# Performance work log

Measured on AMD Instinct MI355X. Metric: run time of the kernel, lower is better.

The kernel has to match this reference:

```python
import jax, jax.numpy as jnp
import numpy as np
from jax import lax

NC = 8  # num_classes
NUM_ITERS = 2


def _resize_bilinear_ac(x, out_h, out_w):
    """Bilinear resize with align_corners=True, x: (N, C, H, W)."""
    N, C, H, W = x.shape

    def coords(n_out, n_in):
        if n_out == 1:
            return jnp.zeros((1,), jnp.float32)
        return jnp.linspace(0.0, float(n_in - 1), n_out, dtype=jnp.float32)

    ys = coords(out_h, H)
    xs = coords(out_w, W)
    y0 = jnp.floor(ys).astype(jnp.int32)
    y1 = jnp.minimum(y0 + 1, H - 1)
    wy = (ys - y0.astype(jnp.float32)).astype(x.dtype)
    x0 = jnp.floor(xs).astype(jnp.int32)
    x1 = jnp.minimum(x0 + 1, W - 1)
    wx = (xs - x0.astype(jnp.float32)).astype(x.dtype)

    r0 = x[:, :, y0, :]
    r1 = x[:, :, y1, :]
    r = r0 * (1.0 - wy)[None, None, :, None] + r1 * wy[None, None, :, None]
    c0 = r[:, :, :, x0]
    c1 = r[:, :, :, x1]
    return c0 * (1.0 - wx)[None, None, None, :] + c1 * wx[None, None, None, :]


def _conv2d(x, w, groups=1):
    k = w.shape[-1]
    pad = k // 2
    return lax.conv_general_dilated(
        x, w, window_strides=(1, 1), padding=[(pad, pad), (pad, pad)],
        dimension_numbers=('NCHW', 'OIHW', 'NCHW'), feature_group_count=groups)


def _mean_field_update(unary, guidance, spatial_w, bilateral_w, compat_w):
    Q = jax.nn.softmax(unary, axis=1)
    cw = compat_w[:, :, 0, 0]  # (O, I)
    for _ in range(NUM_ITERS):
        spatial_msg = _conv2d(Q, spatial_w, groups=NC)          # depthwise 3x3
        bilateral_in = jnp.concatenate([Q, guidance], axis=1)   # (N, NC+6, H, W)
        bilateral_msg = _conv2d(bilateral_in, bilateral_w)      # 3x3 dense
        message = spatial_msg + bilateral_msg
        message = jnp.einsum('nchw,oc->nohw', message, cw)      # 1x1 compat conv
        Q = jax.nn.softmax(unary - message, axis=1)
    return Q


def setup_inputs() -> dict:
    key = jax.random.key(0)
    ks = jax.random.split(key, 16)
    inp = {
        'logits': jax.random.normal(ks[0], (8, NC, 512, 512), jnp.float32),
        'image': jax.random.uniform(ks[1], (8, 3, 512, 512), jnp.float32),
        'skip0': jax.random.normal(ks[2], (8, 64, 256, 256), jnp.float32),
        'skip1': jax.random.normal(ks[3], (8, 128, 128, 128), jnp.float32),
        'skip2': jax.random.normal(ks[4], (8, 256, 64, 64), jnp.float32),
        'skip3': jax.random.normal(ks[5], (8, 512, 32, 32), jnp.float32),
        'spatial_w': jax.random.normal(ks[6], (NC, 1, 3, 3), jnp.float32) * 0.1,
        'bilateral_w': jax.random.normal(ks[7], (NC, NC + 6, 3, 3), jnp.float32) * 0.1,
        # compat_conv is initialized to -I (zeros then -= eye) in the module
        'compat_w': (-jnp.eye(NC, dtype=jnp.float32)).reshape(NC, NC, 1, 1),
        'skip_w0': jax.random.normal(ks[8], (3, 64, 1, 1), jnp.float32) * 0.05,
        'skip_b0': jnp.zeros((3,), jnp.float32),
        'skip_w1': jax.random.normal(ks[9], (3, 128, 1, 1), jnp.float32) * 0.05,
        'skip_b1': jnp.zeros((3,), jnp.float32),
        'skip_w2': jax.random.normal(ks[10], (3, 256, 1, 1), jnp.float32) * 0.05,
        'skip_b2': jnp.zeros((3,), jnp.float32),
        'skip_w3': jax.random.normal(ks[11], (3, 512, 1, 1), jnp.float32) * 0.05,
        'skip_b3': jnp.zeros((3,), jnp.float32),
    }
    return inp


def reference(logits, image, skip0, skip1, skip2, skip3,
              spatial_w, bilateral_w, compat_w,
              skip_w0, skip_b0, skip_w1, skip_b1,
              skip_w2, skip_b2, skip_w3, skip_b3):
    H, W = logits.shape[2], logits.shape[3]

    # fuse_skip_features: 1x1 project each skip to 3ch, upsample, average
    skips = [skip0, skip1, skip2, skip3]
    ws = [skip_w0, skip_w1, skip_w2, skip_w3]
    bs = [skip_b0, skip_b1, skip_b2, skip_b3]
    fused = jnp.zeros((logits.shape[0], 3, H, W), logits.dtype)
    for feat, w, b in zip(skips, ws, bs):
        p = jnp.einsum('nchw,oc->nohw', feat, w[:, :, 0, 0]) + b[None, :, None, None]
        fused = fused + _resize_bilinear_ac(p, H, W)
    fused = fused / len(skips)

    guidance = jnp.concatenate([image, fused], axis=1)  # (N, 6, H, W)

    Q_full = _mean_field_update(logits, guidance, spatial_w, bilateral_w, compat_w)

    logits_down = _resize_bilinear_ac(logits, H // 2, W // 2)
    guidance_down = _resize_bilinear_ac(guidance, H // 2, W // 2)
    Q_down = _mean_field_update(logits_down, guidance_down, spatial_w, bilateral_w, compat_w)
    Q_down_up = _resize_bilinear_ac(Q_down, H, W)

    return (Q_full + Q_down_up) / 2.0
```

## Files before the change

kernel.cpp:

```cpp
#include <hip/hip_runtime.h>
#include <hip/hip_fp16.h>
#include <math.h>

#define NB 8
#define NCLS 8
#define NGU 6
#define NBI 14
#define HF 512
#define WF 512
#define HH 256
#define WH 256

#define TOX 32
#define TOY 16
#define SX 36
#define SY 20
#define SPX (SY * SX)
#define R1W 36
#define R1N (18 * 36)
#define R1T 41
#define R2T 32
#define PLANE (SPX * 8)
#define PSTR (PLANE + 32)
#define TILEH (16 + PSTR + PLANE + 16)

typedef _Float16 f16x8 __attribute__((ext_vector_type(8)));
typedef float f32x4 __attribute__((ext_vector_type(4)));

static __device__ __forceinline__ void ac_prep(int o, float scale, int insz,
                                               int& i0, int& i1, float& f) {
    float s = (float)o * scale;
    int ii = (int)floorf(s);
    if (ii > insz - 1) ii = insz - 1;
    if (ii < 0) ii = 0;
    i0 = ii;
    i1 = (ii + 1 < insz) ? (ii + 1) : (insz - 1);
    f = s - (float)ii;
}

static __device__ __forceinline__ void dma16(const _Float16* g, _Float16* l) {
    __builtin_amdgcn_global_load_lds(
        (const __attribute__((address_space(1))) void*)g,
        (__attribute__((address_space(3))) void*)l, 16, 0, 0);
}

__global__ __launch_bounds__(256) void k_init(
    float* __restrict__ p1, float* __restrict__ p2, float* __restrict__ p3,
    const float* __restrict__ b1, const float* __restrict__ b2, const float* __restrict__ b3,
    const float* __restrict__ wsp, const float* __restrict__ wbil,
    const float* __restrict__ cw, _Float16* __restrict__ wf) {
    int bid = blockIdx.x;
    int tid = threadIdx.x;
    if (bid < 2016) {
        int i = bid * 256 + tid;
        if (i < NB * 3 * 16384) { p1[i] = b1[(i / 16384) % 3]; return; }
        i -= NB * 3 * 16384;
        if (i < NB * 3 * 4096) { p2[i] = b2[(i / 4096) % 3]; return; }
        i -= NB * 3 * 4096;
        p3[i] = b3[(i / 1024) % 3];
        return;
    }
    __shared__ float sW2[NBI * 72];
    for (int i = tid; i < NBI * 72; i += 256) {
        int o = i & 7;
        int t = (i >> 3) % 9;
        int ci = i / 72;
        float s = 0.f;
        for (int c = 0; c < NCLS; ++c)
            s += cw[o * NCLS + c] * wbil[((size_t)c * NBI + ci) * 9 + t];
        if (ci < NCLS) s += cw[o * NCLS + ci] * wsp[ci * 9 + t];
        sW2[i] = s;
    }
    __syncthreads();
    for (int i = tid; i < 5 * 64; i += 256) {
        int l = i & 63;
        int col = l & 15, kg = l >> 4;
        #pragma unroll
        for (int e = 0; e < 8; ++e) {
            int k = (i >> 6) * 32 + kg * 8 + e;
            int tap = k >> 4, ci = k & 15;
            float v = (tap < 9 && ci < 14 && col < 8) ? sW2[ci * 72 + tap * 8 + col] : 0.f;
            wf[i * 8 + e] = (_Float16)v;
        }
    }
}

template <int VEC, int CH, bool DIRECT>
static __device__ __forceinline__ void skip_level(
    const float* __restrict__ feat, const float* __restrict__ sw,
    const float* __restrict__ bias, float* __restrict__ out,
    int C, int HW, int nch, int idx) {
    const int HWv = HW / VEC;
    int hv = idx % HWv;
    int t = idx / HWv;
    int ch = t % nch;
    int n = t / nch;
    int c0 = ch * CH;
    const float* fp = feat + ((size_t)n * C + c0) * HW + (size_t)hv * VEC;
    float a[3][VEC];
    #pragma unroll
    for (int o = 0; o < 3; ++o)
        #pragma unroll
        for (int k = 0; k < VEC; ++k) a[o][k] = 0.f;
    #pragma unroll 8
    for (int c = 0; c < CH; ++c) {
        float v[VEC];
        if constexpr (VEC == 2) {
            float2 t2 = *reinterpret_cast<const float2*>(fp + (size_t)c * HW);
            v[0] = t2.x; v[1] = t2.y;
        } else {
            v[0] = fp[(size_t)c * HW];
        }
        #pragma unroll
        for (int o = 0; o < 3; ++o) {
            const float wv = sw[o * C + c0 + c];
            #pragma unroll
            for (int k = 0; k < VEC; ++k) a[o][k] = fmaf(wv, v[k], a[o][k]);
        }
    }
    float* op = out + (size_t)n * 3 * HW + (size_t)hv * VEC;
    #pragma unroll
    for (int o = 0; o < 3; ++o) {
        #pragma unroll
        for (int k = 0; k < VEC; ++k) {
            if (DIRECT)
                op[(size_t)o * HW + k] = bias[o] + a[o][k];
            else
                atomicAdd(&op[(size_t)o * HW + k], a[o][k]);
        }
    }
}

__global__ __launch_bounds__(256) void k_skip_all(
    const float* __restrict__ s0, const float* __restrict__ s1,
    const float* __restrict__ s2, const float* __restrict__ s3,
    const float* __restrict__ w0, const float* __restrict__ w1,
    const float* __restrict__ w2, const float* __restrict__ w3,
    const float* __restrict__ b0,
    float* __restrict__ p0, float* __restrict__ p1,
    float* __restrict__ p2, float* __restrict__ p3) {
    __shared__ float sw[3 * 512];
    const int bid = blockIdx.x;
    const int lvl = bid >> 10;
    const int idx = (bid & 1023) * 256 + threadIdx.x;
    const float* w = (lvl == 0) ? w0 : (lvl == 1) ? w1 : (lvl == 2) ? w2 : w3;
    const int C = (lvl == 0) ? 64 : (lvl == 1) ? 128 : (lvl == 2) ? 256 : 512;
    for (int i = threadIdx.x; i < 3 * C; i += 256) sw[i] = w[i];
    __syncthreads();
    if (lvl == 0)      skip_level<2, 64, true >(s0, sw, b0, p0, 64, 65536, 1, idx);
    else if (lvl == 1) skip_level<2, 32, false>(s1, sw, nullptr, p1, 128, 16384, 4, idx);
    else if (lvl == 2) skip_level<1, 32, false>(s2, sw, nullptr, p2, 256, 4096, 8, idx);
    else               skip_level<1, 16, false>(s3, sw, nullptr, p3, 512, 1024, 32, idx);
}

__global__ void k_prep_full(const float* __restrict__ logits, const float* __restrict__ image,
                            const float* __restrict__ p0, const float* __restrict__ p1,
                            const float* __restrict__ p2, const float* __restrict__ p3,
                            _Float16* __restrict__ Gh, _Float16* __restrict__ Q0h) {
    const int HW = HF * WF;
    int t = blockIdx.x * blockDim.x + threadIdx.x;
    if (t >= NB * HW / 2) return;
    int idx = t * 2;
    int n = idx / HW, r = idx - n * HW;
    int y = r / WF, x = r - y * WF;

    const float* ps[4] = {p0, p1, p2, p3};
    const int ss[4] = {256, 128, 64, 32};
    float f[2][3] = {{0.f, 0.f, 0.f}, {0.f, 0.f, 0.f}};
    #pragma unroll
    for (int l = 0; l < 4; ++l) {
        int s = ss[l];
        float scale = (float)(s - 1) / 511.0f;
        int y0, y1;
        float fy;
        ac_prep(y, scale, s, y0, y1, fy);
        const float* pb = ps[l] + (size_t)n * 3 * s * s;
        #pragma unroll
        for (int k = 0; k < 2; ++k) {
            int x0, x1;
            float fx;
            ac_prep(x + k, scale, s, x0, x1, fx);
            #pragma unroll
            for (int o = 0; o < 3; ++o) {
                const float* pp = pb + (size_t)o * s * s;
                float v00 = pp[y0 * s + x0], v01 = pp[y0 * s + x1];
                float v10 = pp[y1 * s + x0], v11 = pp[y1 * s + x1];
                float r0 = v00 * (1.f - fy) + v10 * fy;
                float r1 = v01 * (1.f - fy) + v11 * fy;
                f[k][o] += r0 * (1.f - fx) + r1 * fx;
            }
        }
    }
    const float* ip = image + (size_t)n * 3 * HW + r;
    float2 img[3];
    #pragma unroll
    for (int o = 0; o < 3; ++o) img[o] = *reinterpret_cast<const float2*>(&ip[(size_t)o * HW]);
    const float* up = logits + (size_t)n * NCLS * HW + r;
    float2 u[8];
    #pragma unroll
    for (int o = 0; o < 8; ++o) u[o] = *reinterpret_cast<const float2*>(&up[(size_t)o * HW]);

    f16x8 gv[2], qv[2];
    #pragma unroll
    for (int k = 0; k < 2; ++k) {
        gv[k][0] = (_Float16)(k ? img[0].y : img[0].x);
        gv[k][1] = (_Float16)(k ? img[1].y : img[1].x);
        gv[k][2] = (_Float16)(k ? img[2].y : img[2].x);
        gv[k][3] = (_Float16)(f[k][0] * 0.25f);
        gv[k][4] = (_Float16)(f[k][1] * 0.25f);
        gv[k][5] = (_Float16)(f[k][2] * 0.25f);
        gv[k][6] = (_Float16)0.f;
        gv[k][7] = (_Float16)0.f;
        float e[8];
        float s = 0.f;
        #pragma unroll
        for (int o = 0; o < 8; ++o) { e[o] = __expf(k ? u[o].y : u[o].x); s += e[o]; }
        float inv = 1.f / s;
        #pragma unroll
        for (int o = 0; o < 8; ++o) qv[k][o] = (_Float16)(e[o] * inv);
    }
    *(f16x8*)(Gh + (size_t)idx * 8) = gv[0];
    *(f16x8*)(Gh + (size_t)idx * 8 + 8) = gv[1];
    *(f16x8*)(Q0h + (size_t)idx * 8) = qv[0];
    *(f16x8*)(Q0h + (size_t)idx * 8 + 8) = qv[1];
}

template <bool DOWN, bool UPFOLD>
__global__ __launch_bounds__(256, 4) void k_mf_mfma(
    const float* __restrict__ unary, const _Float16* __restrict__ Q0h,
    const _Float16* __restrict__ Gh, const _Float16* __restrict__ Qd,
    void* __restrict__ QoutV, const _Float16* __restrict__ wfragG,
    int H, int W, int Hs, int Ws) {
    __shared__ __align__(16) _Float16 s_t[TILEH];
    __shared__ __align__(16) _Float16 s_msg[R1N * 8];
    _Float16* tb0 = s_t + 16;
    _Float16* tb1 = s_t + 16 + PSTR;

    const int tid = threadIdx.x;
    const int lane = tid & 63;
    const int wv = tid >> 6;
    const int n = blockIdx.z;
    const int gx0 = blockIdx.x * TOX;
    const int gy0 = blockIdx.y * TOY;
    const int HW = H * W;
    const int HWs = Hs * Ws;

    f16x8 wf[5];
    #pragma unroll
    for (int j = 0; j < 5; ++j)
        wf[j] = *(const f16x8*)(wfragG + (j * 64 + lane) * 8);

    if (tid < 16) s_t[tid] = (_Float16)0.f;
    else if (tid < 48) s_t[5760 + tid] = (_Float16)0.f;
    else if (tid < 64) s_t[11520 + tid] = (_Float16)0.f;

    const bool interior = !DOWN && gx0 >= 2 && (gx0 + TOX + 2) <= W &&
                          gy0 >= 2 && (gy0 + TOY + 2) <= H;

    if (!DOWN && interior) {
        const size_t nb = (size_t)n * HW;
        for (int c = wv; c < 12; c += 4) {
            int px = c * 64 + lane;
            int yy = px / SX, xx = px - yy * SX;
            size_t goff = (nb + (size_t)(gy0 + yy - 2) * W + (gx0 + xx - 2)) * 8;
            if (px < SPX) {
                dma16(Q0h + goff, tb0 + (size_t)c * 64 * 8);
                dma16(Gh + goff, tb1 + (size_t)c * 64 * 8);
            }
        }
    } else {
        const float syc = DOWN ? (float)(Hs - 1) / (float)(H - 1) : 1.f;
        const float sxc = DOWN ? (float)(Ws - 1) / (float)(W - 1) : 1.f;
        for (int i = tid; i < SPX; i += 256) {
            int yy = i / SX, xx = i - yy * SX;
            int gy = gy0 + yy - 2, gx = gx0 + xx - 2;
            f16x8 qv, gv;
            #pragma unroll
            for (int o = 0; o < 8; ++o) { qv[o] = (_Float16)0.f; gv[o] = (_Float16)0.f; }
            if ((unsigned)gy < (unsigned)H && (unsigned)gx < (unsigned)W) {
                if (DOWN) {
                    int y0, y1, x0, x1;
                    float fy, fx;
                    ac_prep(gy, syc, Hs, y0, y1, fy);
                    ac_prep(gx, sxc, Ws, x0, x1, fx);
                    const float w00 = (1.f - fy) * (1.f - fx), w01 = (1.f - fy) * fx;
                    const float w10 = fy * (1.f - fx), w11 = fy * fx;
                    const size_t o00 = (size_t)y0 * Ws + x0, o01 = (size_t)y0 * Ws + x1;
                    const size_t o10 = (size_t)y1 * Ws + x0, o11 = (size_t)y1 * Ws + x1;
                    const float* ubase = unary + (size_t)n * NCLS * HWs;
                    float e[8];
                    float s = 0.f;
                    #pragma unroll
                    for (int o = 0; o < 8; ++o) {
                        const float* up = ubase + (size_t)o * HWs;
                        float u = w00 * up[o00] + w01 * up[o01] + w10 * up[o10] + w11 * up[o11];
                        e[o] = __expf(u);
                        s += e[o];
                    }
                    float inv = 1.f / s;
                    #pragma unroll
                    for (int o = 0; o < 8; ++o) qv[o] = (_Float16)(e[o] * inv);
                    const size_t gb = (size_t)n * HWs;
                    f16x8 ga = *(const f16x8*)(Gh + (gb + o00) * 8);
                    f16x8 gb2 = *(const f16x8*)(Gh + (gb + o01) * 8);
                    f16x8 gc = *(const f16x8*)(Gh + (gb + o10) * 8);
                    f16x8 gd = *(const f16x8*)(Gh + (gb + o11) * 8);
                    #pragma unroll
                    for (int c = 0; c < 8; ++c) {
                        float g = w00 * (float)ga[c] + w01 * (float)gb2[c] +
                                  w10 * (float)gc[c] + w11 * (float)gd[c];
                        gv[c] = (_Float16)g;
                    }
                } else {
                    const size_t off = ((size_t)n * HW + (size_t)gy * W + gx) * 8;
                    qv = *(const f16x8*)(Q0h + off);
                    gv = *(const f16x8*)(Gh + off);
                }
            }
            *(f16x8*)(tb0 + i * 8) = qv;
            *(f16x8*)(tb1 + i * 8) = gv;
        }
    }
    __syncthreads();

    for (int t = wv; t < R1T; t += 4) {
        int pb = t * 16;
        int p = pb + (lane & 15);
        if (p > R1N - 1) p = R1N - 1;
        int qy = p / R1W;
        int yy = 1 + qy, xx = p - qy * R1W;
        int kg = lane >> 4;
        f32x4 acc = {0.f, 0.f, 0.f, 0.f};
        #pragma unroll
        for (int j = 0; j < 5; ++j) {
            int tap = 2 * j + (kg >> 1);
            if (tap > 8) tap = 8;
            int dy = tap / 3 - 1, dx = tap - (tap / 3) * 3 - 1;
            int idx = (yy + dy) * SX + (xx + dx);
            f16x8 af = *(const f16x8*)(tb0 + (kg & 1) * PSTR + idx * 8);
            acc = __builtin_amdgcn_mfma_f32_16x16x32_f16(af, wf[j], acc, 0, 0, 0);
        }
        int ch = lane & 15;
        if (ch < 8) {
            int pxb = pb + (lane >> 4) * 4;
            #pragma unroll
            for (int r = 0; r < 4; ++r) {
                int px = pxb + r;
                if (px < R1N) s_msg[px * 8 + ch] = (_Float16)acc[r];
            }
        }
    }
    __syncthreads();

    for (int i = tid; i < R1N; i += 256) {
        int qy = i / R1W;
        int yy = 1 + qy, xx = i - qy * R1W;
        int gy = gy0 + yy - 2, gx = gx0 + xx - 2;
        if (interior || ((unsigned)gy < (unsigned)H && (unsigned)gx < (unsigned)W)) {
            f16x8 m = *(const f16x8*)(s_msg + i * 8);
            f16x8 q0 = *(const f16x8*)(tb0 + (i + SX) * 8);
            float e[8];
            float s = 0.f;
            #pragma unroll
            for (int o = 0; o < 8; ++o) {
                e[o] = (float)q0[o] * __expf(-(float)m[o]);
                s += e[o];
            }
            float inv = 1.f / s;
            f16x8 q1;
            #pragma unroll
            for (int o = 0; o < 8; ++o) q1[o] = (_Float16)(e[o] * inv);
            *(f16x8*)(tb0 + (i + SX) * 8) = q1;
        }
    }
    f16x8 m1r[2];
    #pragma unroll
    for (int u2 = 0; u2 < 2; ++u2) {
        int i = tid + 256 * u2;
        int oy = i >> 5, ox = i & 31;
        int r1 = (1 + oy) * R1W + (2 + ox);
        m1r[u2] = *(const f16x8*)(s_msg + r1 * 8);
    }
    __syncthreads();

    for (int t = wv; t < R2T; t += 4) {
        int pb = t * 16;
        int p = pb + (lane & 15);
        int yy = 2 + (p >> 5), xx = 2 + (p & 31);
        int kg = lane >> 4;
        f32x4 acc = {0.f, 0.f, 0.f, 0.f};
        #pragma unroll
        for (int j = 0; j < 5; ++j) {
            int tap = 2 * j + (kg >> 1);
            if (tap > 8) tap = 8;
            int dy = tap / 3 - 1, dx = tap - (tap / 3) * 3 - 1;
            int idx = (yy + dy) * SX + (xx + dx);
            f16x8 af = *(const f16x8*)(tb0 + (kg & 1) * PSTR + idx * 8);
            acc = __builtin_amdgcn_mfma_f32_16x16x32_f16(af, wf[j], acc, 0, 0, 0);
        }
        int ch = lane & 15;
        if (ch < 8) {
            int pxb = pb + (lane >> 4) * 4;
            #pragma unroll
            for (int r = 0; r < 4; ++r) s_msg[(pxb + r) * 8 + ch] = (_Float16)acc[r];
        }
    }
    __syncthreads();

    #pragma unroll
    for (int u2 = 0; u2 < 2; ++u2) {
        int i = tid + 256 * u2;
        int oy = i >> 5, ox = i & 31;
        int gy = gy0 + oy, gx = gx0 + ox;
        f16x8 m2 = *(const f16x8*)(s_msg + i * 8);
        f16x8 q1 = *(const f16x8*)(tb0 + ((2 + oy) * SX + (2 + ox)) * 8);
        float e[8];
        float s = 0.f;
        #pragma unroll
        for (int o = 0; o < 8; ++o) {
            e[o] = (float)q1[o] * __expf((float)m1r[u2][o] - (float)m2[o]);
            s += e[o];
        }
        float inv = 1.f / s;
        if (UPFOLD) {
            float* qp = (float*)QoutV + (size_t)n * NCLS * HW + (size_t)gy * W + gx;
            int y0, y1, x0, x1;
            float fy, fx;
            ac_prep(gy, 255.f / 511.f, HH, y0, y1, fy);
            ac_prep(gx, 255.f / 511.f, WH, x0, x1, fx);
            const float w00 = (1.f - fy) * (1.f - fx), w01 = (1.f - fy) * fx;
            const float w10 = fy * (1.f - fx), w11 = fy * fx;
            const size_t qb = (size_t)n * (HH * WH);
            f16x8 qa = *(const f16x8*)(Qd + (qb + (size_t)y0 * WH + x0) * 8);
            f16x8 qbv = *(const f16x8*)(Qd + (qb + (size_t)y0 * WH + x1) * 8);
            f16x8 qc = *(const f16x8*)(Qd + (qb + (size_t)y1 * WH + x0) * 8);
            f16x8 qdv = *(const f16x8*)(Qd + (qb + (size_t)y1 * WH + x1) * 8);
            #pragma unroll
            for (int o = 0; o < 8; ++o) {
                float v = w00 * (float)qa[o] + w01 * (float)qbv[o] +
                          w10 * (float)qc[o] + w11 * (float)qdv[o];
                qp[(size_t)o * HW] = fmaf(0.5f, e[o] * inv, 0.5f * v);
            }
        } else {
            _Float16* qo = (_Float16*)QoutV + ((size_t)n * HW + (size_t)gy * W + gx) * 8;
            f16x8 q2;
            #pragma unroll
            for (int o = 0; o < 8; ++o) q2[o] = (_Float16)(e[o] * inv);
            *(f16x8*)qo = q2;
        }
    }
}

static inline int cdiv(int a, int b) { return (a + b - 1) / b; }

extern "C" void kernel_launch(void* const* d_in, const int* in_sizes, int n_in,
                              void* d_out, int out_size, void* d_ws, size_t ws_size,
                              hipStream_t stream) {
    const float* logits = (const float*)d_in[0];
    const float* image = (const float*)d_in[1];
    const float* skip0 = (const float*)d_in[2];
    const float* skip1 = (const float*)d_in[3];
    const float* skip2 = (const float*)d_in[4];
    const float* skip3 = (const float*)d_in[5];
    const float* spatial_w = (const float*)d_in[6];
    const float* bilateral_w = (const float*)d_in[7];
    const float* compat_w = (const float*)d_in[8];
    const float* skip_w0 = (const float*)d_in[9];
    const float* skip_b0 = (const float*)d_in[10];
    const float* skip_w1 = (const float*)d_in[11];
    const float* skip_b1 = (const float*)d_in[12];
    const float* skip_w2 = (const float*)d_in[13];
    const float* skip_b2 = (const float*)d_in[14];
    const float* skip_w3 = (const float*)d_in[15];
    const float* skip_b3 = (const float*)d_in[16];
    float* out = (float*)d_out;
    float* ws = (float*)d_ws;

    float* p0 = ws + 0;
    float* p1 = ws + 1572864;
    float* p2 = ws + 1966080;
    float* p3 = ws + 2064384;
    _Float16* wfrag = (_Float16*)(ws + 2110000);
    _Float16* Q0h = (_Float16*)(ws + 4194304);
    _Float16* Gh = (_Float16*)(ws + 12582912);
    _Float16* Qdh = (_Float16*)(ws + 20971520);

    const int HWf = HF * WF;

    k_init<<<2017, 256, 0, stream>>>(p1, p2, p3, skip_b1, skip_b2, skip_b3,
                                     spatial_w, bilateral_w, compat_w, wfrag);

    k_skip_all<<<4096, 256, 0, stream>>>(skip0, skip1, skip2, skip3,
                                         skip_w0, skip_w1, skip_w2, skip_w3,
                                         skip_b0, p0, p1, p2, p3);

    k_prep_full<<<cdiv(NB * HWf / 2, 256), 256, 0, stream>>>(
        logits, image, p0, p1, p2, p3, Gh, Q0h);

    {
        dim3 grid(WH / TOX, HH / TOY, NB);
        k_mf_mfma<true, false><<<grid, 256, 0, stream>>>(
            logits, nullptr, Gh, nullptr, (void*)Qdh, wfrag, HH, WH, HF, WF);
    }

    {
        dim3 grid(WF / TOX, HF / TOY, NB);
        k_mf_mfma<false, true><<<grid, 256, 0, stream>>>(
            nullptr, Q0h, Gh, Qdh, (void*)out, wfrag, HF, WF, HF, WF);
    }
}
```

Before: 195.1 us.

## Rebalance skip projection split, cut atomics and shrink bias init

Reworks how the 1x1 skip-feature projections are divided across blocks. Level 1 now runs over all channels per thread and writes bias plus result directly, so it no longer needs a bias prefill or atomics. Levels 2 and 3 use fewer channel chunks, and the deep levels are scheduled first. The init kernel now only prefills levels 2 and 3, using float4 stores, which shrinks it from ~2000 blocks to 121. Each thread also issues 8 channel loads at once for more memory-level parallelism. In exchange, per-thread serial work is longer and there are fewer threads for some levels, which may reduce latency hiding.

```diff
diff --git a/kernel.cpp b/kernel.cpp
--- a/kernel.cpp
+++ b/kernel.cpp
@@ -45,19 +45,26 @@
 }
 
 __global__ __launch_bounds__(256) void k_init(
-    float* __restrict__ p1, float* __restrict__ p2, float* __restrict__ p3,
-    const float* __restrict__ b1, const float* __restrict__ b2, const float* __restrict__ b3,
+    float* __restrict__ p2, float* __restrict__ p3,
+    const float* __restrict__ b2, const float* __restrict__ b3,
     const float* __restrict__ wsp, const float* __restrict__ wbil,
     const float* __restrict__ cw, _Float16* __restrict__ wf) {
     int bid = blockIdx.x;
     int tid = threadIdx.x;
-    if (bid < 2016) {
-        int i = bid * 256 + tid;
-        if (i < NB * 3 * 16384) { p1[i] = b1[(i / 16384) % 3]; return; }
-        i -= NB * 3 * 16384;
-        if (i < NB * 3 * 4096) { p2[i] = b2[(i / 4096) % 3]; return; }
-        i -= NB * 3 * 4096;
-        p3[i] = b3[(i / 1024) % 3];
+    if (bid < 120) {
+        int i = (bid * 256 + tid) * 4;
+        float bv;
+        float* dst;
+        if (i < 98304) {
+            bv = b2[(i / 4096) % 3];
+            dst = p2 + i;
+        } else {
+            int j = i - 98304;
+            bv = b3[(j / 1024) % 3];
+            dst = p3 + j;
+        }
+        float4 v = {bv, bv, bv, bv};
+        *reinterpret_cast<float4*>(dst) = v;
         return;
     }
     __shared__ float sW2[NBI * 72];
@@ -85,40 +92,47 @@
     }
 }
 
-template <int VEC, int CH, bool DIRECT>
-static __device__ __forceinline__ void skip_level(
+template <int C, int HW, int NCH, int VEC, bool DIRECT>
+static __device__ __forceinline__ void skip_lvl(
     const float* __restrict__ feat, const float* __restrict__ sw,
-    const float* __restrict__ bias, float* __restrict__ out,
-    int C, int HW, int nch, int idx) {
-    const int HWv = HW / VEC;
-    int hv = idx % HWv;
-    int t = idx / HWv;
-    int ch = t % nch;
-    int n = t / nch;
+    const float* __restrict__ bias, float* __restrict__ out, int idx) {
+    constexpr int CH = C / NCH;
+    constexpr int HWV = HW / VEC;
+    constexpr int PXV = NB * HWV;
+    int pxv = idx % PXV;
+    int ch = idx / PXV;
     int c0 = ch * CH;
-    const float* fp = feat + ((size_t)n * C + c0) * HW + (size_t)hv * VEC;
+    int hwv = pxv % HWV;
+    int n = pxv / HWV;
+    const float* fp = feat + ((size_t)n * C + c0) * HW + (size_t)hwv * VEC;
     float a[3][VEC];
     #pragma unroll
     for (int o = 0; o < 3; ++o)
         #pragma unroll
         for (int k = 0; k < VEC; ++k) a[o][k] = 0.f;
-    #pragma unroll 8
-    for (int c = 0; c < CH; ++c) {
-        float v[VEC];
-        if constexpr (VEC == 2) {
-            float2 t2 = *reinterpret_cast<const float2*>(fp + (size_t)c * HW);
-            v[0] = t2.x; v[1] = t2.y;
-        } else {
-            v[0] = fp[(size_t)c * HW];
-        }
-        #pragma unroll
-        for (int o = 0; o < 3; ++o) {
-            const float wv = sw[o * C + c0 + c];
-            #pragma unroll
-            for (int k = 0; k < VEC; ++k) a[o][k] = fmaf(wv, v[k], a[o][k]);
-        }
-    }
-    float* op = out + (size_t)n * 3 * HW + (size_t)hv * VEC;
+    for (int cb = 0; cb < CH; cb += 8) {
+        float v[8][VEC];
+        #pragma unroll
+        for (int j = 0; j < 8; ++j) {
+            if constexpr (VEC == 2) {
+                float2 t2 = *reinterpret_cast<const float2*>(fp + (size_t)(cb + j) * HW);
+                v[j][0] = t2.x;
+                v[j][1] = t2.y;
+            } else {
+                v[j][0] = fp[(size_t)(cb + j) * HW];
+            }
+        }
+        #pragma unroll
+        for (int j = 0; j < 8; ++j) {
+            #pragma unroll
+            for (int o = 0; o < 3; ++o) {
+                const float wv = sw[o * C + c0 + cb + j];
+                #pragma unroll
+                for (int k = 0; k < VEC; ++k) a[o][k] = fmaf(wv, v[j][k], a[o][k]);
+            }
+        }
+    }
+    float* op = out + (size_t)n * 3 * HW + (size_t)hwv * VEC;
     #pragma unroll
     for (int o = 0; o < 3; ++o) {
         #pragma unroll
@@ -136,21 +150,26 @@
     const float* __restrict__ s2, const float* __restrict__ s3,
     const float* __restrict__ w0, const float* __restrict__ w1,
     const float* __restrict__ w2, const float* __restrict__ w3,
-    const float* __restrict__ b0,
+    const float* __restrict__ b0, const float* __restrict__ b1,
     float* __restrict__ p0, float* __restrict__ p1,
     float* __restrict__ p2, float* __restrict__ p3) {
     __shared__ float sw[3 * 512];
     const int bid = blockIdx.x;
-    const int lvl = bid >> 10;
-    const int idx = (bid & 1023) * 256 + threadIdx.x;
+    const int tid = threadIdx.x;
+    int lvl, base;
+    if (bid < 128) { lvl = 3; base = 0; }
+    else if (bid < 384) { lvl = 2; base = 128; }
+    else if (bid < 640) { lvl = 1; base = 384; }
+    else { lvl = 0; base = 640; }
     const float* w = (lvl == 0) ? w0 : (lvl == 1) ? w1 : (lvl == 2) ? w2 : w3;
     const int C = (lvl == 0) ? 64 : (lvl == 1) ? 128 : (lvl == 2) ? 256 : 512;
-    for (int i = threadIdx.x; i < 3 * C; i += 256) sw[i] = w[i];
+    for (int i = tid; i < 3 * C; i += 256) sw[i] = w[i];
     __syncthreads();
-    if (lvl == 0)      skip_level<2, 64, true >(s0, sw, b0, p0, 64, 65536, 1, idx);
-    else if (lvl == 1) skip_level<2, 32, false>(s1, sw, nullptr, p1, 128, 16384, 4, idx);
-    else if (lvl == 2) skip_level<1, 32, false>(s2, sw, nullptr, p2, 256, 4096, 8, idx);
-    else               skip_level<1, 16, false>(s3, sw, nullptr, p3, 512, 1024, 32, idx);
+    const int idx = (bid - base) * 256 + tid;
+    if (lvl == 3)      skip_lvl<512, 1024, 4, 1, false>(s3, sw, nullptr, p3, idx);
+    else if (lvl == 2) skip_lvl<256, 4096, 2, 1, false>(s2, sw, nullptr, p2, idx);
+    else if (lvl == 1) skip_lvl<128, 16384, 1, 2, true>(s1, sw, b1, p1, idx);
+    else               skip_lvl<64, 65536, 1, 2, true>(s0, sw, b0, p0, idx);
 }
 
 __global__ void k_prep_full(const float* __restrict__ logits, const float* __restrict__ image,
@@ -487,12 +506,12 @@
 
     const int HWf = HF * WF;
 
-    k_init<<<2017, 256, 0, stream>>>(p1, p2, p3, skip_b1, skip_b2, skip_b3,
-                                     spatial_w, bilateral_w, compat_w, wfrag);
-
-    k_skip_all<<<4096, 256, 0, stream>>>(skip0, skip1, skip2, skip3,
+    k_init<<<121, 256, 0, stream>>>(p2, p3, skip_b2, skip_b3,
+                                    spatial_w, bilateral_w, compat_w, wfrag);
+
+    k_skip_all<<<1664, 256, 0, stream>>>(skip0, skip1, skip2, skip3,
                                          skip_w0, skip_w1, skip_w2, skip_w3,
-                                         skip_b0, p0, p1, p2, p3);
+                                         skip_b0, skip_b1, p0, p1, p2, p3);
 
     k_prep_full<<<cdiv(NB * HWf / 2, 256), 256, 0, stream>>>(
         logits, image, p0, p1, p2, p3, Gh, Q0h);
```

Measured after the change: 195.1 us. Within noise of the previous version (+0.0%).
